# Optimization experiments

Hardware: AMD Instinct MI355X
Metric: run time of the kernel (lower is better)

The kernel has to match this reference:

```python
import jax, jax.numpy as jnp
import numpy as np

D_MODEL = 1024
NUM_HEADS = 16
HEAD_DIM = D_MODEL // NUM_HEADS


def setup_inputs() -> dict:
    key = jax.random.key(0)
    k0, k1, k2, k3, k4 = jax.random.split(key, 5)
    B, S, D = 4, 2048, D_MODEL
    std = np.sqrt(2.0 / (D + D)).astype(np.float32)
    return {
        "in_features": jax.random.normal(k0, (B, S, D), dtype=jnp.float32),
        "Wq": jax.random.normal(k1, (D, D), dtype=jnp.float32) * std,
        "Wk": jax.random.normal(k2, (D, D), dtype=jnp.float32) * std,
        "Wv": jax.random.normal(k3, (D, D), dtype=jnp.float32) * std,
        "Wo": jax.random.normal(k4, (D, D), dtype=jnp.float32) * std,
    }


def reference(in_features, Wq, Wk, Wv, Wo):
    B, S, D = in_features.shape
    H, Hd = NUM_HEADS, HEAD_DIM

    def split_heads(x):  # (B,S,D) -> (B,H,S,Hd)
        return x.reshape(B, S, H, Hd).transpose(0, 2, 1, 3)

    q = split_heads(in_features @ Wq.T)
    k = split_heads(in_features @ Wk.T)
    v = split_heads(in_features @ Wv.T)

    scale = 1.0 / jnp.sqrt(jnp.asarray(Hd, dtype=q.dtype))
    scores = jnp.einsum("bhsd,bhtd->bhst", q, k) * scale  # (B,H,S,S)
    causal = jnp.tril(jnp.ones((S, S), dtype=bool))  # (S,S)
    scores = jnp.where(causal[None, None], scores, -jnp.inf)
    attn = jax.nn.softmax(scores, axis=-1)
    out = jnp.einsum("bhst,bhtd->bhsd", attn, v)  # (B,H,S,Hd)
    out = out.transpose(0, 2, 1, 3).reshape(B, S, D)
    return out @ Wo.T
```

## Files before the change

### kernel.cpp

```cpp
#include <hip/hip_runtime.h>


typedef float f32x4 __attribute__((ext_vector_type(4)));
typedef float f32x16 __attribute__((ext_vector_type(16)));
typedef short s16x8 __attribute__((ext_vector_type(8)));

#if __has_builtin(__builtin_amdgcn_exp2f)
#define EXP2(x) __builtin_amdgcn_exp2f(x)
#else
#define EXP2(x) exp2f(x)
#endif

__device__ __forceinline__ unsigned short f2bf(float f) {
  unsigned int u = __float_as_uint(f);
  u += 0x7fffu + ((u >> 16) & 1u);
  return (unsigned short)(u >> 16);
}

__device__ __forceinline__ unsigned int pk2bf(float f0, float f1) {
  return __builtin_amdgcn_perm(__float_as_uint(f1) + 0x8000u,
                               __float_as_uint(f0) + 0x8000u, 0x07060302u);
}

__device__ __forceinline__ unsigned int pk2bf_t(float f0, float f1) {
  return __builtin_amdgcn_perm(__float_as_uint(f1), __float_as_uint(f0), 0x07060302u);
}

__device__ __forceinline__ void gl_lds16(const short* g, short* lds) {
  __builtin_amdgcn_global_load_lds(
      (const __attribute__((address_space(1))) unsigned int*)g,
      (__attribute__((address_space(3))) unsigned int*)lds, 16, 0, 0);
}

__global__ __launch_bounds__(256) void cvt_all(const float4* __restrict__ X,
                                               const float4* __restrict__ Wq,
                                               const float4* __restrict__ Wk,
                                               const float4* __restrict__ Wv,
                                               const float4* __restrict__ Wo,
                                               ushort4* __restrict__ xb,
                                               ushort4* __restrict__ wqkv,
                                               ushort4* __restrict__ wob) {
  const int NX = 8192 * 1024 / 4;
  const int NW = 1024 * 1024 / 4;
  const int NT = NX + 4 * NW;
  int i = blockIdx.x * blockDim.x + threadIdx.x;
  int stride = gridDim.x * blockDim.x;
  for (int idx = i; idx < NT; idx += stride) {
    const float4* s;
    ushort4* d;
    int off;
    if (idx < NX) {
      s = X; d = xb; off = idx;
    } else {
      int j = idx - NX;
      int w = j >> 18;
      off = j & (NW - 1);
      switch (w) {
        case 0: s = Wq; d = wqkv; break;
        case 1: s = Wk; d = wqkv + NW; break;
        case 2: s = Wv; d = wqkv + 2 * NW; break;
        default: s = Wo; d = wob; break;
      }
    }
    float4 f = s[off];
    ushort4 r;
    r.x = f2bf(f.x); r.y = f2bf(f.y); r.z = f2bf(f.z); r.w = f2bf(f.w);
    d[off] = r;
  }
}

template <int MODE>
__global__ __launch_bounds__(256) void gemm_bt(const short* __restrict__ A,
                                               const short* __restrict__ B,
                                               float* __restrict__ Cf,
                                               short* __restrict__ q_o,
                                               short* __restrict__ k_o,
                                               short* __restrict__ vT_o,
                                               int M, int N, int K) {
  const int tid = threadIdx.x;
  const int wave = tid >> 6, lane = tid & 63;
  const int quad = lane >> 4, l15 = lane & 15;
  const int m0 = blockIdx.x * 128, n0 = blockIdx.y * 128;
  const int wm = (wave >> 1) * 64, wn = (wave & 1) * 64;

  __shared__ __align__(16) short As[128 * 64];
  __shared__ __align__(16) short Bs[128 * 64];

  const f32x4 z4 = {0.f, 0.f, 0.f, 0.f};
  f32x4 acc[4][4];
  for (int i = 0; i < 4; ++i)
    for (int j = 0; j < 4; ++j) acc[i][j] = z4;

  for (int k0 = 0; k0 < K; k0 += 64) {
    __syncthreads();
    for (int i = 0; i < 4; ++i) {
      int c = wave * 4 + i;
      int r = c * 8 + (lane >> 3);
      int c8 = (lane & 7) ^ (r & 7);
      gl_lds16(A + (size_t)(m0 + r) * K + k0 + c8 * 8, As + c * 512 + lane * 8);
      gl_lds16(B + (size_t)(n0 + r) * K + k0 + c8 * 8, Bs + c * 512 + lane * 8);
    }
    __syncthreads();
    for (int kk = 0; kk < 64; kk += 32) {
      int c8b = (kk >> 3) + quad;
      s16x8 af[4], bfr[4];
      for (int mt = 0; mt < 4; ++mt) {
        int row = wm + mt * 16 + l15;
        af[mt] = *(const s16x8*)(As + row * 64 + ((c8b ^ (row & 7)) << 3));
      }
      for (int nt = 0; nt < 4; ++nt) {
        int row = wn + nt * 16 + l15;
        bfr[nt] = *(const s16x8*)(Bs + row * 64 + ((c8b ^ (row & 7)) << 3));
      }
      for (int mt = 0; mt < 4; ++mt)
        for (int nt = 0; nt < 4; ++nt)
          acc[mt][nt] = __builtin_amdgcn_mfma_f32_16x16x32_bf16(af[mt], bfr[nt],
                                                                acc[mt][nt], 0, 0, 0);
    }
  }

  if (MODE == 0) {
    for (int mt = 0; mt < 4; ++mt)
      for (int nt = 0; nt < 4; ++nt) {
        int col = n0 + wn + nt * 16 + l15;
        for (int r = 0; r < 4; ++r) {
          int row = m0 + wm + mt * 16 + quad * 4 + r;
          Cf[(size_t)row * N + col] = acc[mt][nt][r];
        }
      }
  } else {
    if (n0 < 1024) {
      const float scale = 0.18033688011112042f;
      for (int mt = 0; mt < 4; ++mt)
        for (int nt = 0; nt < 4; ++nt) {
          int col = n0 + wn + nt * 16 + l15;
          for (int r = 0; r < 4; ++r) {
            int row = m0 + wm + mt * 16 + quad * 4 + r;
            ((unsigned short*)q_o)[(size_t)row * 1024 + col] = f2bf(acc[mt][nt][r] * scale);
          }
        }
    } else if (n0 < 2048) {
      for (int mt = 0; mt < 4; ++mt)
        for (int nt = 0; nt < 4; ++nt) {
          int col = n0 - 1024 + wn + nt * 16 + l15;
          for (int r = 0; r < 4; ++r) {
            int row = m0 + wm + mt * 16 + quad * 4 + r;
            ((unsigned short*)k_o)[(size_t)row * 1024 + col] = f2bf(acc[mt][nt][r]);
          }
        }
    } else {
      for (int mt = 0; mt < 4; ++mt)
        for (int nt = 0; nt < 4; ++nt) {
          int col = n0 - 2048 + wn + nt * 16 + l15;
          int h = col >> 6, d = col & 63;
          int row0 = m0 + wm + mt * 16 + quad * 4;
          int b = row0 >> 11, s = row0 & 2047;
          uint2 pk;
          pk.x = pk2bf(acc[mt][nt][0], acc[mt][nt][1]);
          pk.y = pk2bf(acc[mt][nt][2], acc[mt][nt][3]);
          *(uint2*)((unsigned short*)vT_o + (((size_t)b * 16 + h) * 64 + d) * 2048 + s) = pk;
        }
    }
  }
}

__global__ __launch_bounds__(256, 2) void attn_kernel(const short* __restrict__ qb,
                                                      const short* __restrict__ kb,
                                                      const short* __restrict__ vT,
                                                      short* __restrict__ ob) {
  const int bh = blockIdx.x;
  const int qt = 15 - (int)blockIdx.y;
  const int tid = threadIdx.x;
  const int wave = tid >> 6, lane = tid & 63;
  const int l31 = lane & 31, h = lane >> 5;
  const int q0 = qt * 128;
  const size_t rowbase = (size_t)(bh >> 4) * 2048;
  const int hoff = (bh & 15) * 64;

  __shared__ __align__(16) short Ks[2][8192];
  __shared__ __align__(16) short VTs[2][8192];

  const int kc = wave * 4;
  const int kr = kc * 8 + (lane >> 3);
  const short* ksrc = kb + (rowbase + kr) * 1024 + hoff + (((lane & 7) ^ (kr & 7)) << 3);
  const int vg = lane & 15;
  const short* vsrc_i[4];
#pragma unroll
  for (int i = 0; i < 4; ++i) {
    int d = (kc + i) * 4 + (lane >> 4);
    vsrc_i[i] = vT + ((size_t)bh * 64 + d) * 2048 + ((vg ^ (d & 7)) << 3);
  }

  s16x8 qf[4];
  {
    const short* qrow = qb + (rowbase + q0 + wave * 32 + l31) * 1024 + hoff + h * 8;
#pragma unroll
    for (int k = 0; k < 4; ++k) qf[k] = *(const s16x8*)(qrow + k * 16);
  }

#pragma unroll
  for (int i = 0; i < 4; ++i)
    gl_lds16(ksrc + i * 8 * 1024, Ks[0] + (kc + i) * 512 + lane * 8);
#pragma unroll
  for (int i = 0; i < 4; ++i)
    gl_lds16(vsrc_i[i], VTs[0] + (kc + i) * 512 + lane * 8);

  f32x16 oacc[2];
#pragma unroll
  for (int dt = 0; dt < 2; ++dt)
#pragma unroll
    for (int e = 0; e < 16; ++e) oacc[dt][e] = 0.f;
  float lacc = 0.f;
  const int kswz = l31 & 7;

  for (int t = 0; t <= qt; ++t) {
    __syncthreads();
    const int cur = t & 1;

    if (t < qt) {
      const int nxt = cur ^ 1;
      const short* ks = ksrc + (size_t)(t + 1) * 128 * 1024;
#pragma unroll
      for (int i = 0; i < 4; ++i)
        gl_lds16(ks + i * 8 * 1024, Ks[nxt] + (kc + i) * 512 + lane * 8);
#pragma unroll
      for (int i = 0; i < 4; ++i)
        gl_lds16(vsrc_i[i] + (t + 1) * 128, VTs[nxt] + (kc + i) * 512 + lane * 8);
    }

    const short* Kc = Ks[cur];
    const short* Vc = VTs[cur];

    unsigned int pp[4][8];
    float sum = 0.f;
#pragma unroll
    for (int g = 0; g < 2; ++g) {
      f32x16 s0, s1;
#pragma unroll
      for (int e = 0; e < 16; ++e) { s0[e] = 0.f; s1[e] = 0.f; }
#pragma unroll
      for (int ks = 0; ks < 4; ++ks) {
        int pos = ((ks << 1) + h) ^ kswz;
        s16x8 kf0 = *(const s16x8*)(Kc + ((2 * g) * 32 + l31) * 64 + (pos << 3));
        s16x8 kf1 = *(const s16x8*)(Kc + ((2 * g + 1) * 32 + l31) * 64 + (pos << 3));
        s0 = __builtin_amdgcn_mfma_f32_32x32x16_bf16(kf0, qf[ks], s0, 0, 0, 0);
        s1 = __builtin_amdgcn_mfma_f32_32x32x16_bf16(kf1, qf[ks], s1, 0, 0, 0);
      }
      if (t == qt) {
        int qg = wave * 32 + l31;
#pragma unroll
        for (int e = 0; e < 16; ++e) {
          int rloc = (e & 3) + 8 * (e >> 2) + 4 * h;
          if ((2 * g) * 32 + rloc > qg) s0[e] = -1e30f;
          if ((2 * g + 1) * 32 + rloc > qg) s1[e] = -1e30f;
        }
      }
#pragma unroll
      for (int rg = 0; rg < 8; ++rg) {
        float a0 = EXP2(s0[2 * rg]), a1 = EXP2(s0[2 * rg + 1]);
        float b0 = EXP2(s1[2 * rg]), b1 = EXP2(s1[2 * rg + 1]);
        sum += (a0 + a1) + (b0 + b1);
        pp[2 * g][rg] = pk2bf_t(a0, a1);
        pp[2 * g + 1][rg] = pk2bf_t(b0, b1);
      }
    }
    lacc += sum;

#pragma unroll
    for (int s = 0; s < 8; ++s) {
      int m = s >> 1, base = (s & 1) * 4;
      unsigned int ax = pp[m][base + 0], ay = pp[m][base + 1];
      unsigned int bx = pp[m][base + 2], by = pp[m][base + 3];
      unsigned int sx = h ? ax : bx, sy = h ? ay : by;
      unsigned int rx = (unsigned int)__shfl_xor((int)sx, 32);
      unsigned int ry = (unsigned int)__shfl_xor((int)sy, 32);
      union { s16x8 v; unsigned int u[4]; } pf;
      pf.u[0] = h ? rx : ax;
      pf.u[1] = h ? ry : ay;
      pf.u[2] = h ? bx : rx;
      pf.u[3] = h ? by : ry;
#pragma unroll
      for (int dt = 0; dt < 2; ++dt) {
        int d = dt * 32 + l31;
        s16x8 vf = *(const s16x8*)(Vc + d * 128 + ((((s << 1) + h) ^ (d & 7)) << 3));
        oacc[dt] = __builtin_amdgcn_mfma_f32_32x32x16_bf16(vf, pf.v, oacc[dt], 0, 0, 0);
      }
    }
  }

  lacc += __shfl_xor(lacc, 32);
  float inv = 1.0f / lacc;
  size_t row = rowbase + q0 + wave * 32 + l31;
  unsigned short* orow = (unsigned short*)ob + row * 1024 + hoff;
#pragma unroll
  for (int dt = 0; dt < 2; ++dt)
#pragma unroll
    for (int rg = 0; rg < 4; ++rg) {
      int d = dt * 32 + rg * 8 + 4 * h;
      uint2 pk;
      pk.x = pk2bf(oacc[dt][rg * 4 + 0] * inv, oacc[dt][rg * 4 + 1] * inv);
      pk.y = pk2bf(oacc[dt][rg * 4 + 2] * inv, oacc[dt][rg * 4 + 3] * inv);
      *(uint2*)(orow + d) = pk;
    }
}

extern "C" void kernel_launch(void* const* d_in, const int* in_sizes, int n_in,
                              void* d_out, int out_size, void* d_ws, size_t ws_size,
                              hipStream_t stream) {
  const float* X  = (const float*)d_in[0];
  const float* Wq = (const float*)d_in[1];
  const float* Wk = (const float*)d_in[2];
  const float* Wv = (const float*)d_in[3];
  const float* Wo = (const float*)d_in[4];

  short* xb   = (short*)d_ws;
  short* wqkv = xb + (size_t)8192 * 1024;
  short* wob  = wqkv + (size_t)3072 * 1024;
  short* qb   = wob + (size_t)1024 * 1024;
  short* kb   = qb + (size_t)8192 * 1024;
  short* vT   = kb + (size_t)8192 * 1024;
  short* ob   = xb;

  const int MB = 8192;

  cvt_all<<<3072, 256, 0, stream>>>((const float4*)X, (const float4*)Wq, (const float4*)Wk,
                                    (const float4*)Wv, (const float4*)Wo, (ushort4*)xb,
                                    (ushort4*)wqkv, (ushort4*)wob);

  gemm_bt<1><<<dim3(64, 24), 256, 0, stream>>>(xb, wqkv, nullptr, qb, kb, vT, MB, 3072, 1024);

  attn_kernel<<<dim3(64, 16), 256, 0, stream>>>(qb, kb, vT, ob);

  gemm_bt<0><<<dim3(64, 8), 256, 0, stream>>>(ob, wob, (float*)d_out, nullptr, nullptr,
                                              nullptr, MB, 1024, 1024);
}
```

Before: 236.6 us.

## Replace QKV GEMM with 256x256-tile 8-wave double-buffered pipelined kernel

Adds a dedicated QKV projection kernel using 256x256 tiles with 512 threads. It double-buffers LDS with staged global-to-LDS loads interleaved between four MFMA quadrant phases, and uses setprio around the MFMA blocks. An XCD-aware block remapping improves L2 locality. The aim is to raise MFMA utilization and hide load latency compared to the single-buffered 128x128 kernel. The cost is more LDS (128KB per block) and more register pressure, plus hand-written waitcnt ordering that could be fragile.

New measurement: 238.2 us. Within noise of the previous version (+0.7%).

```diff
diff --git a/kernel.cpp b/kernel.cpp
--- a/kernel.cpp
+++ b/kernel.cpp
@@ -10,6 +10,8 @@
 #else
 #define EXP2(x) exp2f(x)
 #endif
+
+#define MFMA16(a, b, c) __builtin_amdgcn_mfma_f32_16x16x32_bf16(a, b, c, 0, 0, 0)
 
 __device__ __forceinline__ unsigned short f2bf(float f) {
   unsigned int u = __float_as_uint(f);
@@ -69,6 +71,223 @@
   }
 }
 
+__global__ __launch_bounds__(512, 2) void gemm_qkv(const short* __restrict__ A,
+                                                   const short* __restrict__ B,
+                                                   short* __restrict__ q_o,
+                                                   short* __restrict__ k_o,
+                                                   short* __restrict__ vT_o,
+                                                   int M, int N, int K) {
+  const int tid = threadIdx.x;
+  const int lane = tid & 63;
+  const int wave = tid >> 6;
+  const int quad = lane >> 4, l15 = lane & 15;
+  const int wm = wave >> 2, wn = wave & 3;
+
+  const int ny = N >> 8;
+  const int nwg = gridDim.x;
+  const int o = blockIdx.x;
+  const int q8 = nwg >> 3, r8 = nwg & 7;
+  const int xcd = o & 7, idx = o >> 3;
+  const int wg = (xcd < r8 ? xcd * (q8 + 1) : r8 * (q8 + 1) + (xcd - r8) * q8) + idx;
+  const int bx = wg / ny, by = wg - bx * ny;
+  const int m0 = bx << 8, n0 = by << 8;
+
+  __shared__ __align__(16) short As[2][256 * 64];
+  __shared__ __align__(16) short Bs[2][256 * 64];
+
+  const int NK = K >> 6;
+
+  const int sr = tid >> 3;
+  const int c8s = (tid & 7) ^ (sr & 7);
+  const short* a0 = A + (size_t)(m0 + sr) * K + c8s * 8;
+  const short* b0 = B + (size_t)(n0 + sr) * K + c8s * 8;
+  short* adst = &As[0][0] + tid * 8;
+  short* bdst = &Bs[0][0] + tid * 8;
+  const size_t rs64 = (size_t)64 * K;
+
+#define STG_A(buf, t, half)                                                          \
+  {                                                                                  \
+    gl_lds16(a0 + (2 * (half)) * rs64 + (size_t)(t) * 64,                            \
+             adst + (buf) * 16384 + (2 * (half)) * 4096);                            \
+    gl_lds16(a0 + (2 * (half) + 1) * rs64 + (size_t)(t) * 64,                        \
+             adst + (buf) * 16384 + (2 * (half) + 1) * 4096);                        \
+  }
+#define STG_B(buf, t, half)                                                          \
+  {                                                                                  \
+    gl_lds16(b0 + (2 * (half)) * rs64 + (size_t)(t) * 64,                            \
+             bdst + (buf) * 16384 + (2 * (half)) * 4096);                            \
+    gl_lds16(b0 + (2 * (half) + 1) * rs64 + (size_t)(t) * 64,                        \
+             bdst + (buf) * 16384 + (2 * (half) + 1) * 4096);                        \
+  }
+
+  const short* Ab = &As[0][0];
+  const short* Bb = &Bs[0][0];
+  auto rdA = [&](int buf, int row, int ks) -> s16x8 {
+    return *(const s16x8*)(Ab + buf * 16384 + row * 64 + ((((ks << 2) + quad) ^ (row & 7)) << 3));
+  };
+  auto rdB = [&](int buf, int row, int ks) -> s16x8 {
+    return *(const s16x8*)(Bb + buf * 16384 + row * 64 + ((((ks << 2) + quad) ^ (row & 7)) << 3));
+  };
+
+  const f32x4 z4 = {0.f, 0.f, 0.f, 0.f};
+  f32x4 acc[8][4];
+#pragma unroll
+  for (int i = 0; i < 8; ++i)
+#pragma unroll
+    for (int j = 0; j < 4; ++j) acc[i][j] = z4;
+
+  STG_A(0, 0, 0); STG_A(0, 0, 1); STG_B(0, 0, 0); STG_B(0, 0, 1);
+  if (NK > 1) {
+    STG_A(1, 1, 0); STG_B(1, 1, 1);
+    asm volatile("s_waitcnt vmcnt(4)" ::: "memory");
+  } else {
+    asm volatile("s_waitcnt vmcnt(0)" ::: "memory");
+  }
+  __builtin_amdgcn_s_barrier();
+
+  for (int t = 0; t < NK; ++t) {
+    const int bt = t & 1, bn = bt ^ 1;
+    s16x8 af[4][2], bf[2][2], bg[2][2];
+
+#pragma unroll
+    for (int m = 0; m < 4; ++m) {
+      const int row = wm * 64 + m * 16 + l15;
+      af[m][0] = rdA(bt, row, 0);
+      af[m][1] = rdA(bt, row, 1);
+    }
+#pragma unroll
+    for (int n = 0; n < 2; ++n) {
+      const int row = wn * 32 + n * 16 + l15;
+      bf[n][0] = rdB(bt, row, 0);
+      bf[n][1] = rdB(bt, row, 1);
+    }
+    if (t + 1 < NK) STG_A(bn, t + 1, 1);
+    __builtin_amdgcn_s_barrier();
+    asm volatile("s_waitcnt lgkmcnt(0)" ::: "memory");
+    __builtin_amdgcn_sched_barrier(0);
+    __builtin_amdgcn_s_setprio(1);
+#pragma unroll
+    for (int m = 0; m < 4; ++m)
+#pragma unroll
+      for (int n = 0; n < 2; ++n) {
+        acc[m][n] = MFMA16(af[m][0], bf[n][0], acc[m][n]);
+        acc[m][n] = MFMA16(af[m][1], bf[n][1], acc[m][n]);
+      }
+    __builtin_amdgcn_s_setprio(0);
+    __builtin_amdgcn_s_barrier();
+
+#pragma unroll
+    for (int n = 0; n < 2; ++n) {
+      const int row = 128 + wn * 32 + n * 16 + l15;
+      bg[n][0] = rdB(bt, row, 0);
+      bg[n][1] = rdB(bt, row, 1);
+    }
+    if (t + 1 < NK) STG_B(bn, t + 1, 0);
+    __builtin_amdgcn_s_barrier();
+    asm volatile("s_waitcnt lgkmcnt(0)" ::: "memory");
+    __builtin_amdgcn_sched_barrier(0);
+    __builtin_amdgcn_s_setprio(1);
+#pragma unroll
+    for (int m = 0; m < 4; ++m)
+#pragma unroll
+      for (int n = 0; n < 2; ++n) {
+        acc[m][2 + n] = MFMA16(af[m][0], bg[n][0], acc[m][2 + n]);
+        acc[m][2 + n] = MFMA16(af[m][1], bg[n][1], acc[m][2 + n]);
+      }
+    __builtin_amdgcn_s_setprio(0);
+    __builtin_amdgcn_s_barrier();
+
+#pragma unroll
+    for (int m = 0; m < 4; ++m) {
+      const int row = 128 + wm * 64 + m * 16 + l15;
+      af[m][0] = rdA(bt, row, 0);
+      af[m][1] = rdA(bt, row, 1);
+    }
+    if (t + 2 < NK) STG_A(bt, t + 2, 0);
+    __builtin_amdgcn_s_barrier();
+    asm volatile("s_waitcnt lgkmcnt(0)" ::: "memory");
+    __builtin_amdgcn_sched_barrier(0);
+    __builtin_amdgcn_s_setprio(1);
+#pragma unroll
+    for (int m = 0; m < 4; ++m)
+#pragma unroll
+      for (int n = 0; n < 2; ++n) {
+        acc[4 + m][2 + n] = MFMA16(af[m][0], bg[n][0], acc[4 + m][2 + n]);
+        acc[4 + m][2 + n] = MFMA16(af[m][1], bg[n][1], acc[4 + m][2 + n]);
+      }
+    __builtin_amdgcn_s_setprio(0);
+    __builtin_amdgcn_s_barrier();
+
+#pragma unroll
+    for (int n = 0; n < 2; ++n) {
+      const int row = wn * 32 + n * 16 + l15;
+      bf[n][0] = rdB(bt, row, 0);
+      bf[n][1] = rdB(bt, row, 1);
+    }
+    if (t + 2 < NK) STG_B(bt, t + 2, 1);
+    __builtin_amdgcn_s_barrier();
+    asm volatile("s_waitcnt lgkmcnt(0)" ::: "memory");
+    __builtin_amdgcn_sched_barrier(0);
+    __builtin_amdgcn_s_setprio(1);
+#pragma unroll
+    for (int m = 0; m < 4; ++m)
+#pragma unroll
+      for (int n = 0; n < 2; ++n) {
+        acc[4 + m][n] = MFMA16(af[m][0], bf[n][0], acc[4 + m][n]);
+        acc[4 + m][n] = MFMA16(af[m][1], bf[n][1], acc[4 + m][n]);
+      }
+    __builtin_amdgcn_s_setprio(0);
+    if (t + 2 < NK) {
+      asm volatile("s_waitcnt vmcnt(4)" ::: "memory");
+    } else {
+      asm volatile("s_waitcnt vmcnt(0)" ::: "memory");
+    }
+    __builtin_amdgcn_sched_barrier(0);
+    __builtin_amdgcn_s_barrier();
+  }
+#undef STG_A
+#undef STG_B
+
+  if (by < 4) {
+    const float scale = 0.18033688011112042f;
+#pragma unroll
+    for (int mt = 0; mt < 8; ++mt)
+#pragma unroll
+      for (int nt = 0; nt < 4; ++nt) {
+        const int col = n0 + (nt >> 1) * 128 + wn * 32 + (nt & 1) * 16 + l15;
+        const int row0 = m0 + (mt >> 2) * 128 + wm * 64 + (mt & 3) * 16 + quad * 4;
+#pragma unroll
+        for (int r = 0; r < 4; ++r)
+          ((unsigned short*)q_o)[(size_t)(row0 + r) * 1024 + col] = f2bf(acc[mt][nt][r] * scale);
+      }
+  } else if (by < 8) {
+#pragma unroll
+    for (int mt = 0; mt < 8; ++mt)
+#pragma unroll
+      for (int nt = 0; nt < 4; ++nt) {
+        const int col = n0 - 1024 + (nt >> 1) * 128 + wn * 32 + (nt & 1) * 16 + l15;
+        const int row0 = m0 + (mt >> 2) * 128 + wm * 64 + (mt & 3) * 16 + quad * 4;
+#pragma unroll
+        for (int r = 0; r < 4; ++r)
+          ((unsigned short*)k_o)[(size_t)(row0 + r) * 1024 + col] = f2bf(acc[mt][nt][r]);
+      }
+  } else {
+#pragma unroll
+    for (int mt = 0; mt < 8; ++mt)
+#pragma unroll
+      for (int nt = 0; nt < 4; ++nt) {
+        const int col = n0 - 2048 + (nt >> 1) * 128 + wn * 32 + (nt & 1) * 16 + l15;
+        const int h = col >> 6, d = col & 63;
+        const int row0 = m0 + (mt >> 2) * 128 + wm * 64 + (mt & 3) * 16 + quad * 4;
+        const int b = row0 >> 11, s = row0 & 2047;
+        uint2 pk;
+        pk.x = pk2bf(acc[mt][nt][0], acc[mt][nt][1]);
+        pk.y = pk2bf(acc[mt][nt][2], acc[mt][nt][3]);
+        *(uint2*)((unsigned short*)vT_o + (((size_t)b * 16 + h) * 64 + d) * 2048 + s) = pk;
+      }
+  }
+}
+
 template <int MODE>
 __global__ __launch_bounds__(256) void gemm_bt(const short* __restrict__ A,
                                                const short* __restrict__ B,
@@ -114,8 +333,7 @@
       }
       for (int mt = 0; mt < 4; ++mt)
         for (int nt = 0; nt < 4; ++nt)
-          acc[mt][nt] = __builtin_amdgcn_mfma_f32_16x16x32_bf16(af[mt], bfr[nt],
-                                                                acc[mt][nt], 0, 0, 0);
+          acc[mt][nt] = MFMA16(af[mt], bfr[nt], acc[mt][nt]);
     }
   }
 
@@ -128,39 +346,6 @@
           Cf[(size_t)row * N + col] = acc[mt][nt][r];
         }
       }
-  } else {
-    if (n0 < 1024) {
-      const float scale = 0.18033688011112042f;
-      for (int mt = 0; mt < 4; ++mt)
-        for (int nt = 0; nt < 4; ++nt) {
-          int col = n0 + wn + nt * 16 + l15;
-          for (int r = 0; r < 4; ++r) {
-            int row = m0 + wm + mt * 16 + quad * 4 + r;
-            ((unsigned short*)q_o)[(size_t)row * 1024 + col] = f2bf(acc[mt][nt][r] * scale);
-          }
-        }
-    } else if (n0 < 2048) {
-      for (int mt = 0; mt < 4; ++mt)
-        for (int nt = 0; nt < 4; ++nt) {
-          int col = n0 - 1024 + wn + nt * 16 + l15;
-          for (int r = 0; r < 4; ++r) {
-            int row = m0 + wm + mt * 16 + quad * 4 + r;
-            ((unsigned short*)k_o)[(size_t)row * 1024 + col] = f2bf(acc[mt][nt][r]);
-          }
-        }
-    } else {
-      for (int mt = 0; mt < 4; ++mt)
-        for (int nt = 0; nt < 4; ++nt) {
-          int col = n0 - 2048 + wn + nt * 16 + l15;
-          int h = col >> 6, d = col & 63;
-          int row0 = m0 + wm + mt * 16 + quad * 4;
-          int b = row0 >> 11, s = row0 & 2047;
-          uint2 pk;
-          pk.x = pk2bf(acc[mt][nt][0], acc[mt][nt][1]);
-          pk.y = pk2bf(acc[mt][nt][2], acc[mt][nt][3]);
-          *(uint2*)((unsigned short*)vT_o + (((size_t)b * 16 + h) * 64 + d) * 2048 + s) = pk;
-        }
-    }
   }
 }
 
@@ -327,7 +512,7 @@
                                     (const float4*)Wv, (const float4*)Wo, (ushort4*)xb,
                                     (ushort4*)wqkv, (ushort4*)wob);
 
-  gemm_bt<1><<<dim3(64, 24), 256, 0, stream>>>(xb, wqkv, nullptr, qb, kb, vT, MB, 3072, 1024);
+  gemm_qkv<<<dim3(384), dim3(512), 0, stream>>>(xb, wqkv, qb, kb, vT, MB, 3072, 1024);
 
   attn_kernel<<<dim3(64, 16), 256, 0, stream>>>(qb, kb, vT, ob);
 
```
